# Kernel optimization log

Hardware: AMD Instinct MI355X
Metric: run time of the kernel (lower is better)

## Reference

```python
import jax, jax.numpy as jnp
import numpy as np

B, C, H, W = 4, 256, 128, 128
OUT = 50

def setup_inputs() -> dict:
    key = jax.random.key(0)
    k1, k2, k3 = jax.random.split(key, 3)
    x = jax.random.normal(k1, (B, C, H, W), dtype=jnp.float32)
    # conv2d 1x1 weights, kaiming-ish scale
    W_f = jax.random.normal(k2, (OUT, C), dtype=jnp.float32) * (1.0 / np.sqrt(C))
    W_beta = jax.random.normal(k3, (C, C), dtype=jnp.float32) * (1.0 / np.sqrt(C))
    return {"x": x, "W_f": W_f, "W_beta": W_beta}

def reference(x, W_f, W_beta):
    b, c, h, w = x.shape
    n = h * w
    xf = x.reshape(b, c, n)                      # [B,C,N]
    F = jnp.einsum('oc,bcn->bon', W_f, xf)       # 1x1 conv -> [B,O,N]
    # S = softmax(F @ A, axis over C), A = xf^T : [B,N,C]
    S = jnp.einsum('bon,bcn->boc', F, xf)        # [B,O,C]
    S = jax.nn.softmax(S, axis=2)
    St = jnp.swapaxes(S, 1, 2)                   # [B,C,O]
    E = jnp.einsum('bco,bon->bcn', St, F)        # [B,C,N]
    E = E.reshape(b, c, h, w)
    E = jnp.einsum('dc,bchw->bdhw', W_beta, E) + x  # beta conv + residual
    return E
```

## Files before the change

kernel.cpp:

```cpp
#include <hip/hip_runtime.h>
#include <math.h>

#define CCH 256
#define OCH 50
#define NPIX 16384
#define BATCH 4
#define BO (BATCH*OCH)
#define NSPLIT2 256
#define KC2 (NPIX/NSPLIT2)

typedef _Float16 f16x8 __attribute__((ext_vector_type(8)));
typedef float f32x4 __attribute__((ext_vector_type(4)));
typedef unsigned int uint;
typedef unsigned short ushort;

__device__ __forceinline__ void cvt_split(const float4 v0, const float4 v1,
                                          f16x8& h, f16x8& l) {
    float v[8] = {v0.x, v0.y, v0.z, v0.w, v1.x, v1.y, v1.z, v1.w};
#pragma unroll
    for (int j = 0; j < 8; ++j) {
        _Float16 hj = (_Float16)v[j];
        h[j] = hj;
        l[j] = (_Float16)(v[j] - (float)hj);
    }
}

__device__ __forceinline__ uint packhl(float v) {
    _Float16 h = (_Float16)v;
    _Float16 l = (_Float16)(v - (float)h);
    union { _Float16 f; ushort u; } H, L;
    H.f = h; L.f = l;
    return (uint)H.u | ((uint)L.u << 16);
}

__device__ __forceinline__ void unpack8(const uint* w, f16x8& h, f16x8& l) {
    union { uint u[4]; f16x8 v; } H, L;
#pragma unroll
    for (int k = 0; k < 4; ++k) {
        H.u[k] = __builtin_amdgcn_perm(w[2 * k + 1], w[2 * k], 0x05040100u);
        L.u[k] = __builtin_amdgcn_perm(w[2 * k + 1], w[2 * k], 0x07060302u);
    }
    h = H.v; l = L.v;
}

__global__ void k0_pack(const float* __restrict__ Wf, uint* __restrict__ Wf16p) {
    int i = blockIdx.x * 256 + threadIdx.x;
    if (i < 64 * CCH) {
        int o = i / CCH;
        float v = (o < OCH) ? Wf[i] : 0.f;
        Wf16p[i] = packhl(v);
    }
}

__global__ __launch_bounds__(256) void k1_mfma(const float* __restrict__ x,
                                               const uint* __restrict__ Wf16p,
                                               float* __restrict__ F) {
    int b  = blockIdx.y;
    int p0 = blockIdx.x * 64;
    int t  = threadIdx.x;
    int w = t >> 6, lane = t & 63, r16 = lane & 15, kg = lane >> 4;
    __shared__ uint xl[2][32 * 64];

    int cidx = t & 15;
    int pixg = t >> 4;
    const float* xb = x + ((size_t)b * CCH) * NPIX + p0;

    float4 r0 = *(const float4*)(xb + (size_t)cidx * NPIX + pixg * 4);
    float4 r1 = *(const float4*)(xb + (size_t)(16 + cidx) * NPIX + pixg * 4);

    f32x4 acc[4];
#pragma unroll
    for (int nt = 0; nt < 4; ++nt) acc[nt] = {0.f, 0.f, 0.f, 0.f};

    const uint* Arow = Wf16p + (w * 16 + r16) * CCH;

    {
        float v0[4] = {r0.x, r0.y, r0.z, r0.w};
        float v1[4] = {r1.x, r1.y, r1.z, r1.w};
#pragma unroll
        for (int j = 0; j < 4; ++j) {
            int pix = pixg * 4 + j;
            int q = (pix & 7) << 2;
            xl[0][pix * 32 + (cidx ^ q)]        = packhl(v0[j]);
            xl[0][pix * 32 + ((16 + cidx) ^ q)] = packhl(v1[j]);
        }
    }
    __syncthreads();

#pragma unroll
    for (int s = 0; s < 8; ++s) {
        if (s < 7) {
            r0 = *(const float4*)(xb + (size_t)((s + 1) * 32 + cidx) * NPIX + pixg * 4);
            r1 = *(const float4*)(xb + (size_t)((s + 1) * 32 + 16 + cidx) * NPIX + pixg * 4);
        }
        uint aw[8];
        *(uint4*)aw       = *(const uint4*)(Arow + s * 32 + kg * 8);
        *(uint4*)(aw + 4) = *(const uint4*)(Arow + s * 32 + kg * 8 + 4);
        f16x8 Ah, Al;
        unpack8(aw, Ah, Al);

        const uint* buf = xl[s & 1];
#pragma unroll
        for (int nt = 0; nt < 4; ++nt) {
            int pix = nt * 16 + r16;
            int q = (r16 & 7) << 2;
            uint bw[8];
            *(uint4*)bw       = *(const uint4*)&buf[pix * 32 + ((kg * 8) ^ q)];
            *(uint4*)(bw + 4) = *(const uint4*)&buf[pix * 32 + ((kg * 8 + 4) ^ q)];
            f16x8 Bh, Bl;
            unpack8(bw, Bh, Bl);
            acc[nt] = __builtin_amdgcn_mfma_f32_16x16x32_f16(Ah, Bh, acc[nt], 0, 0, 0);
            acc[nt] = __builtin_amdgcn_mfma_f32_16x16x32_f16(Ah, Bl, acc[nt], 0, 0, 0);
            acc[nt] = __builtin_amdgcn_mfma_f32_16x16x32_f16(Al, Bh, acc[nt], 0, 0, 0);
        }
        if (s < 7) {
            float v0[4] = {r0.x, r0.y, r0.z, r0.w};
            float v1[4] = {r1.x, r1.y, r1.z, r1.w};
            uint* nbuf = xl[(s + 1) & 1];
#pragma unroll
            for (int j = 0; j < 4; ++j) {
                int pix = pixg * 4 + j;
                int q = (pix & 7) << 2;
                nbuf[pix * 32 + (cidx ^ q)]        = packhl(v0[j]);
                nbuf[pix * 32 + ((16 + cidx) ^ q)] = packhl(v1[j]);
            }
            __syncthreads();
        }
    }

    float* Fb = F + ((size_t)b * 64 + w * 16 + kg * 4) * NPIX + p0;
#pragma unroll
    for (int nt = 0; nt < 4; ++nt)
#pragma unroll
        for (int r = 0; r < 4; ++r)
            Fb[(size_t)r * NPIX + nt * 16 + r16] = acc[nt][r];
}

__global__ __launch_bounds__(256) void k2_mfma(const float* __restrict__ x,
                                               const float* __restrict__ F,
                                               float* __restrict__ Spart) {
    int ks = blockIdx.x;
    int b  = blockIdx.y;
    int ch = blockIdx.z;
    int wave = threadIdx.x >> 6;
    int lane = threadIdx.x & 63;
    int r16  = lane & 15;
    int kg   = lane >> 4;
    int n0   = ks * KC2;

    const float* Ab = F + ((size_t)b * 64 + wave * 16 + r16) * NPIX + n0 + kg * 8;
    f16x8 Ah0, Al0, Ah1, Al1;
    cvt_split(*(const float4*)Ab, *(const float4*)(Ab + 4), Ah0, Al0);
    cvt_split(*(const float4*)(Ab + 32), *(const float4*)(Ab + 36), Ah1, Al1);

    const float* Bb = x + ((size_t)b * CCH + ch * 128 + r16) * NPIX + n0 + kg * 8;
    float4 c0 = *(const float4*)(Bb);
    float4 c1 = *(const float4*)(Bb + 4);
    float4 c2 = *(const float4*)(Bb + 32);
    float4 c3 = *(const float4*)(Bb + 36);

    f32x4 acc[8];
#pragma unroll
    for (int nt = 0; nt < 8; ++nt) acc[nt] = {0.f, 0.f, 0.f, 0.f};

#pragma unroll
    for (int nt = 0; nt < 8; ++nt) {
        float4 p0_, p1_, p2_, p3_;
        if (nt < 7) {
            const float* bp = Bb + (size_t)(nt + 1) * 16 * NPIX;
            p0_ = *(const float4*)(bp);
            p1_ = *(const float4*)(bp + 4);
            p2_ = *(const float4*)(bp + 32);
            p3_ = *(const float4*)(bp + 36);
        }
        f16x8 bh, bl;
        cvt_split(c0, c1, bh, bl);
        acc[nt] = __builtin_amdgcn_mfma_f32_16x16x32_f16(Ah0, bh, acc[nt], 0, 0, 0);
        acc[nt] = __builtin_amdgcn_mfma_f32_16x16x32_f16(Ah0, bl, acc[nt], 0, 0, 0);
        acc[nt] = __builtin_amdgcn_mfma_f32_16x16x32_f16(Al0, bh, acc[nt], 0, 0, 0);
        cvt_split(c2, c3, bh, bl);
        acc[nt] = __builtin_amdgcn_mfma_f32_16x16x32_f16(Ah1, bh, acc[nt], 0, 0, 0);
        acc[nt] = __builtin_amdgcn_mfma_f32_16x16x32_f16(Ah1, bl, acc[nt], 0, 0, 0);
        acc[nt] = __builtin_amdgcn_mfma_f32_16x16x32_f16(Al1, bh, acc[nt], 0, 0, 0);
        if (nt < 7) { c0 = p0_; c1 = p1_; c2 = p2_; c3 = p3_; }
    }
    float* Sp = Spart + (((size_t)ks * BATCH + b) * 64 + wave * 16 + kg * 4) * 256
              + ch * 128 + r16;
#pragma unroll
    for (int nt = 0; nt < 8; ++nt)
#pragma unroll
        for (int r = 0; r < 4; ++r)
            Sp[(size_t)r * 256 + nt * 16] = acc[nt][r];
}

__global__ __launch_bounds__(1024) void k2r_softmax(const float* __restrict__ Spart,
                                                    float* __restrict__ S) {
    int row = blockIdx.x;
    int b = row / OCH, o = row % OCH;
    int tid = threadIdx.x;
    int c = tid & 255, g = tid >> 8;
    __shared__ float part[4][CCH];
    __shared__ float red[8];
    float v = 0.f;
    const size_t ksStride = (size_t)BATCH * 64 * 256;
    const float* p = Spart + ((size_t)(g * (NSPLIT2 / 4)) * BATCH + b) * 64 * 256
                   + (size_t)o * 256 + c;
#pragma unroll 8
    for (int ks = 0; ks < NSPLIT2 / 4; ++ks)
        v += p[ks * ksStride];
    part[g][c] = v;
    __syncthreads();
    float vv = 0.f, e = 0.f, m;
    if (tid < 256) {
        vv = part[0][c] + part[1][c] + part[2][c] + part[3][c];
        m = vv;
#pragma unroll
        for (int off = 32; off > 0; off >>= 1) m = fmaxf(m, __shfl_xor(m, off, 64));
        if ((tid & 63) == 0) red[tid >> 6] = m;
    }
    __syncthreads();
    if (tid < 256) {
        m = fmaxf(fmaxf(red[0], red[1]), fmaxf(red[2], red[3]));
        e = expf(vv - m);
        float s = e;
#pragma unroll
        for (int off = 32; off > 0; off >>= 1) s += __shfl_xor(s, off, 64);
        if ((tid & 63) == 0) red[4 + (tid >> 6)] = s;
    }
    __syncthreads();
    if (tid < 256) {
        float tot = red[4] + red[5] + red[6] + red[7];
        S[(size_t)row * CCH + c] = e / tot;
    }
}

__global__ __launch_bounds__(256) void k3_M(const float* __restrict__ Wbeta,
                                            const float* __restrict__ S,
                                            float* __restrict__ Mt) {
    int row = blockIdx.x;
    int d = threadIdx.x;
    const float* srow = S + (size_t)row * CCH;
    const float4* wb = (const float4*)(Wbeta + (size_t)d * CCH);
    float acc = 0.f;
#pragma unroll 4
    for (int cg = 0; cg < CCH / 4; ++cg) {
        float4 w = wb[cg];
        float4 s = *(const float4*)(srow + cg * 4);
        acc += w.x * s.x + w.y * s.y + w.z * s.z + w.w * s.w;
    }
    Mt[(size_t)row * CCH + d] = acc;
}

__global__ __launch_bounds__(256) void k4_out(const float* __restrict__ x,
                                              const float* __restrict__ F,
                                              const float* __restrict__ Mt,
                                              float* __restrict__ out) {
    int b  = blockIdx.z;
    int dq = blockIdx.y;
    int n  = blockIdx.x * 256 + threadIdx.x;
    float acc[32];
#pragma unroll
    for (int dd = 0; dd < 32; ++dd) acc[dd] = 0.f;
    const float* Fp = F + (size_t)b * 64 * NPIX + n;
    const float* mt = Mt + (size_t)b * OCH * CCH + dq * 32;
#pragma unroll 2
    for (int o = 0; o < OCH; ++o) {
        float fo = Fp[(size_t)o * NPIX];
        const float* m = mt + o * CCH;
#pragma unroll
        for (int dd = 0; dd < 32; ++dd) acc[dd] = fmaf(m[dd], fo, acc[dd]);
    }
    const float* xp = x + ((size_t)b * CCH + dq * 32) * NPIX + n;
    float* op = out + ((size_t)b * CCH + dq * 32) * NPIX + n;
#pragma unroll
    for (int dd = 0; dd < 32; ++dd)
        __builtin_nontemporal_store(acc[dd] + xp[(size_t)dd * NPIX], &op[(size_t)dd * NPIX]);
}

extern "C" void kernel_launch(void* const* d_in, const int* in_sizes, int n_in,
                              void* d_out, int out_size, void* d_ws, size_t ws_size,
                              hipStream_t stream) {
    const float* x     = (const float*)d_in[0];
    const float* Wf    = (const float*)d_in[1];
    const float* Wbeta = (const float*)d_in[2];
    float* out = (float*)d_out;

    float* F     = (float*)d_ws;
    uint*  Wf16p = (uint*)(F + (size_t)BATCH * 64 * NPIX);
    float* S     = (float*)(Wf16p + 64 * CCH);
    float* Mt    = S + (size_t)BO * CCH;
    float* Spart = out;

    k0_pack<<<dim3((64 * CCH + 255) / 256), dim3(256), 0, stream>>>(Wf, Wf16p);
    k1_mfma<<<dim3(NPIX / 64, BATCH), dim3(256), 0, stream>>>(x, Wf16p, F);
    k2_mfma<<<dim3(NSPLIT2, BATCH, 2), dim3(256), 0, stream>>>(x, F, Spart);
    k2r_softmax<<<dim3(BO), dim3(1024), 0, stream>>>(Spart, S);
    k3_M<<<dim3(BO), dim3(256), 0, stream>>>(Wbeta, S, Mt);
    k4_out<<<dim3(NPIX / 256, 8, BATCH), dim3(256), 0, stream>>>(x, F, Mt, out);
}
```

Baseline: 202.2 us.

## Fuse 1x1 conv GEMM and F·x^T partial GEMM into one kernel via LDS

Merges the kernel computing F = W_f·x with the kernel computing the partial S = F·x^T per 64-pixel chunk. Each block keeps its freshly computed F tile in shared memory and feeds it straight into the second MFMA stage, so the second stage no longer reads F back from global memory, and one launch is removed. x for the chunk is re-read from global (likely from cache) for the second stage. This adds LDS usage and a launch-bounds occupancy hint, and the block count for the second stage halves because both channel halves are now handled in one block.

Result: faster. 193.8 us (-4.1%).

```diff
diff --git a/kernel.cpp b/kernel.cpp
--- a/kernel.cpp
+++ b/kernel.cpp
@@ -52,14 +52,17 @@
     }
 }
 
-__global__ __launch_bounds__(256) void k1_mfma(const float* __restrict__ x,
-                                               const uint* __restrict__ Wf16p,
-                                               float* __restrict__ F) {
+__global__ __launch_bounds__(256, 4) void k12_mfma(const float* __restrict__ x,
+                                                   const uint* __restrict__ Wf16p,
+                                                   float* __restrict__ F,
+                                                   float* __restrict__ Spart) {
     int b  = blockIdx.y;
-    int p0 = blockIdx.x * 64;
+    int ks = blockIdx.x;
+    int p0 = ks * KC2;
     int t  = threadIdx.x;
     int w = t >> 6, lane = t & 63, r16 = lane & 15, kg = lane >> 4;
     __shared__ uint xl[2][32 * 64];
+    __shared__ float Ft[4][16 * 68];
 
     int cidx = t & 15;
     int pixg = t >> 4;
@@ -134,63 +137,50 @@
 #pragma unroll
         for (int r = 0; r < 4; ++r)
             Fb[(size_t)r * NPIX + nt * 16 + r16] = acc[nt][r];
-}
-
-__global__ __launch_bounds__(256) void k2_mfma(const float* __restrict__ x,
-                                               const float* __restrict__ F,
-                                               float* __restrict__ Spart) {
-    int ks = blockIdx.x;
-    int b  = blockIdx.y;
-    int ch = blockIdx.z;
-    int wave = threadIdx.x >> 6;
-    int lane = threadIdx.x & 63;
-    int r16  = lane & 15;
-    int kg   = lane >> 4;
-    int n0   = ks * KC2;
-
-    const float* Ab = F + ((size_t)b * 64 + wave * 16 + r16) * NPIX + n0 + kg * 8;
+
+    float* ft = Ft[w];
+#pragma unroll
+    for (int nt = 0; nt < 4; ++nt)
+#pragma unroll
+        for (int r = 0; r < 4; ++r)
+            ft[(kg * 4 + r) * 68 + nt * 16 + r16] = acc[nt][r];
+    __syncthreads();
+
     f16x8 Ah0, Al0, Ah1, Al1;
-    cvt_split(*(const float4*)Ab, *(const float4*)(Ab + 4), Ah0, Al0);
-    cvt_split(*(const float4*)(Ab + 32), *(const float4*)(Ab + 36), Ah1, Al1);
-
-    const float* Bb = x + ((size_t)b * CCH + ch * 128 + r16) * NPIX + n0 + kg * 8;
-    float4 c0 = *(const float4*)(Bb);
-    float4 c1 = *(const float4*)(Bb + 4);
-    float4 c2 = *(const float4*)(Bb + 32);
-    float4 c3 = *(const float4*)(Bb + 36);
-
-    f32x4 acc[8];
-#pragma unroll
-    for (int nt = 0; nt < 8; ++nt) acc[nt] = {0.f, 0.f, 0.f, 0.f};
-
-#pragma unroll
-    for (int nt = 0; nt < 8; ++nt) {
-        float4 p0_, p1_, p2_, p3_;
-        if (nt < 7) {
-            const float* bp = Bb + (size_t)(nt + 1) * 16 * NPIX;
-            p0_ = *(const float4*)(bp);
-            p1_ = *(const float4*)(bp + 4);
-            p2_ = *(const float4*)(bp + 32);
-            p3_ = *(const float4*)(bp + 36);
-        }
-        f16x8 bh, bl;
-        cvt_split(c0, c1, bh, bl);
-        acc[nt] = __builtin_amdgcn_mfma_f32_16x16x32_f16(Ah0, bh, acc[nt], 0, 0, 0);
-        acc[nt] = __builtin_amdgcn_mfma_f32_16x16x32_f16(Ah0, bl, acc[nt], 0, 0, 0);
-        acc[nt] = __builtin_amdgcn_mfma_f32_16x16x32_f16(Al0, bh, acc[nt], 0, 0, 0);
-        cvt_split(c2, c3, bh, bl);
-        acc[nt] = __builtin_amdgcn_mfma_f32_16x16x32_f16(Ah1, bh, acc[nt], 0, 0, 0);
-        acc[nt] = __builtin_amdgcn_mfma_f32_16x16x32_f16(Ah1, bl, acc[nt], 0, 0, 0);
-        acc[nt] = __builtin_amdgcn_mfma_f32_16x16x32_f16(Al1, bh, acc[nt], 0, 0, 0);
-        if (nt < 7) { c0 = p0_; c1 = p1_; c2 = p2_; c3 = p3_; }
-    }
-    float* Sp = Spart + (((size_t)ks * BATCH + b) * 64 + wave * 16 + kg * 4) * 256
-              + ch * 128 + r16;
-#pragma unroll
-    for (int nt = 0; nt < 8; ++nt)
-#pragma unroll
-        for (int r = 0; r < 4; ++r)
-            Sp[(size_t)r * 256 + nt * 16] = acc[nt][r];
+    {
+        const float* fr = ft + r16 * 68;
+        cvt_split(*(const float4*)(fr + kg * 8), *(const float4*)(fr + kg * 8 + 4), Ah0, Al0);
+        cvt_split(*(const float4*)(fr + 32 + kg * 8), *(const float4*)(fr + 32 + kg * 8 + 4), Ah1, Al1);
+    }
+
+    const float* Bb = x + ((size_t)b * CCH) * NPIX + p0 + kg * 8;
+#pragma unroll
+    for (int half = 0; half < 2; ++half) {
+        f32x4 sacc[8];
+#pragma unroll
+        for (int i = 0; i < 8; ++i) sacc[i] = {0.f, 0.f, 0.f, 0.f};
+#pragma unroll
+        for (int ct = 0; ct < 8; ++ct) {
+            int c = (half * 8 + ct) * 16 + r16;
+            const float* bp = Bb + (size_t)c * NPIX;
+            f16x8 bh, bl;
+            cvt_split(*(const float4*)bp, *(const float4*)(bp + 4), bh, bl);
+            sacc[ct] = __builtin_amdgcn_mfma_f32_16x16x32_f16(Ah0, bh, sacc[ct], 0, 0, 0);
+            sacc[ct] = __builtin_amdgcn_mfma_f32_16x16x32_f16(Ah0, bl, sacc[ct], 0, 0, 0);
+            sacc[ct] = __builtin_amdgcn_mfma_f32_16x16x32_f16(Al0, bh, sacc[ct], 0, 0, 0);
+            cvt_split(*(const float4*)(bp + 32), *(const float4*)(bp + 36), bh, bl);
+            sacc[ct] = __builtin_amdgcn_mfma_f32_16x16x32_f16(Ah1, bh, sacc[ct], 0, 0, 0);
+            sacc[ct] = __builtin_amdgcn_mfma_f32_16x16x32_f16(Ah1, bl, sacc[ct], 0, 0, 0);
+            sacc[ct] = __builtin_amdgcn_mfma_f32_16x16x32_f16(Al1, bh, sacc[ct], 0, 0, 0);
+        }
+        float* Sp = Spart + (((size_t)ks * BATCH + b) * 64 + w * 16 + kg * 4) * 256
+                  + half * 128 + r16;
+#pragma unroll
+        for (int ct = 0; ct < 8; ++ct)
+#pragma unroll
+            for (int r = 0; r < 4; ++r)
+                Sp[(size_t)r * 256 + ct * 16] = sacc[ct][r];
+    }
 }
 
 __global__ __launch_bounds__(1024) void k2r_softmax(const float* __restrict__ Spart,
@@ -292,8 +282,7 @@
     float* Spart = out;
 
     k0_pack<<<dim3((64 * CCH + 255) / 256), dim3(256), 0, stream>>>(Wf, Wf16p);
-    k1_mfma<<<dim3(NPIX / 64, BATCH), dim3(256), 0, stream>>>(x, Wf16p, F);
-    k2_mfma<<<dim3(NSPLIT2, BATCH, 2), dim3(256), 0, stream>>>(x, F, Spart);
+    k12_mfma<<<dim3(NSPLIT2, BATCH), dim3(256), 0, stream>>>(x, Wf16p, F, Spart);
     k2r_softmax<<<dim3(BO), dim3(1024), 0, stream>>>(Spart, S);
     k3_M<<<dim3(BO), dim3(256), 0, stream>>>(Wbeta, S, Mt);
     k4_out<<<dim3(NPIX / 256, 8, BATCH), dim3(256), 0, stream>>>(x, F, Mt, out);
```
